# Optimization experiments

Measured on AMD Instinct MI355X. Metric: run time of the kernel, lower is better.

Reference implementation:

```python
import jax, jax.numpy as jnp
import numpy as np

D_MODEL = 1024
STATE_DIM = 256
BATCH = 4
SEQ_LEN = 4096


def setup_inputs() -> dict:
    key = jax.random.key(0)
    k_u, k_B, k_C = jax.random.split(key, 3)
    u = jax.random.normal(k_u, (BATCH, SEQ_LEN, D_MODEL), dtype=jnp.float32)
    # parameters (as in torch init)
    log_lambda = jnp.linspace(2.94, 4.6, STATE_DIM, dtype=jnp.float32)
    # nn.Linear weight shape is [out_features, in_features]
    B_w = jax.random.normal(k_B, (STATE_DIM, D_MODEL), dtype=jnp.float32) / np.sqrt(D_MODEL)
    C_w = jax.random.normal(k_C, (D_MODEL, STATE_DIM), dtype=jnp.float32) / np.sqrt(STATE_DIM)
    D = jnp.ones((D_MODEL,), dtype=jnp.float32)
    return {"u": u, "log_lambda": log_lambda, "B_w": B_w, "C_w": C_w, "D": D}


def reference(u, log_lambda, B_w, C_w, D):
    batch, seq_len, d = u.shape
    # Bu = B(u): [B, L, N]
    Bu = jnp.einsum("bld,nd->bln", u, B_w)
    lam = jax.nn.sigmoid(log_lambda)                     # [N]
    t = jnp.arange(seq_len, dtype=lam.dtype)
    kernel = lam[None, :] ** t[:, None]                  # [L, N]
    # next power of two >= 2*L (static)
    fft_len = 1
    while fft_len < 2 * seq_len:
        fft_len *= 2
    K_hat = jnp.fft.rfft(kernel, n=fft_len, axis=0)      # [F, N]
    Bu_hat = jnp.fft.rfft(Bu, n=fft_len, axis=1)         # [B, F, N]
    h_hat = K_hat[None, :, :] * Bu_hat
    h = jnp.fft.irfft(h_hat, n=fft_len, axis=1)[:, :seq_len, :]  # [B, L, N]
    y = jnp.einsum("bln,dn->bld", h, C_w) + D * u
    return y
```

## Files before the change

kernel.cpp:

```cpp
#include <hip/hip_runtime.h>
#include <hip/hip_bf16.h>

#define D_MODEL 1024
#define STATE_N 256
#define BATCH 4
#define SEQ_LEN 4096
#define M_TOTAL (BATCH * SEQ_LEN)
#define NCHUNK 128
#define CHUNK (SEQ_LEN / NCHUNK)

typedef __attribute__((ext_vector_type(8))) short bf16x8;
typedef __attribute__((ext_vector_type(4))) short s16x4;
typedef __attribute__((ext_vector_type(4))) float f32x4;

static __device__ inline short f2bf(float f) {
    union { float f; unsigned u; } v; v.f = f;
    unsigned r = v.u + 0x7FFFu + ((v.u >> 16) & 1u);
    return (short)(r >> 16);
}
static __device__ inline float bf2f(short s) {
    union { unsigned u; float f; } v;
    v.u = ((unsigned)(unsigned short)s) << 16;
    return v.f;
}
static __device__ inline float sigmoidf(float x) { return 1.0f / (1.0f + expf(-x)); }

#define GLOAD_LDS16(gp, lp)                                                     \
    __builtin_amdgcn_global_load_lds(                                           \
        (const __attribute__((address_space(1))) void*)(gp),                    \
        (__attribute__((address_space(3))) void*)(lp), 16, 0, 0)

#define WAITVM(N) asm volatile("s_waitcnt vmcnt(" #N ")" ::: "memory")
#define WAITLGKM0 asm volatile("s_waitcnt lgkmcnt(0)" ::: "memory")
#define BARRIER() do { __builtin_amdgcn_s_barrier(); asm volatile("" ::: "memory"); } while (0)

__global__ void prep(const float* __restrict__ Bw, const float* __restrict__ Cw,
                     const float* __restrict__ ll,
                     short* __restrict__ Bwt, short* __restrict__ Cwt,
                     float* __restrict__ W) {
    const int bx = blockIdx.x, tid = threadIdx.x;
    if (bx >= 256) {
        const int i = bx - 256, n = tid;
        W[i * 256 + n] = powf(sigmoidf(ll[n]), (float)(31 - i));
        return;
    }
    const int g = bx * 256 + tid;
    const float* s; short* d;
    if (g < 32768) {
        const int col = g & 127, kc = (g >> 7) & 7, kt = (g >> 10) & 15, cb = g >> 14;
        s = Bw + (size_t)(cb * 128 + col) * D_MODEL + kt * 64 + kc * 8;
        d = Bwt + (size_t)g * 8;
    } else {
        const int h = g - 32768;
        const int col = h & 63, ksq = (h >> 6) & 7, tt = (h >> 9) & 3, cb = h >> 11;
        s = Cw + (size_t)(cb * 64 + col) * STATE_N + tt * 64 + ksq * 8;
        d = Cwt + (size_t)h * 8;
    }
    const f32x4 v0 = *(const f32x4*)s;
    const f32x4 v1 = *(const f32x4*)(s + 4);
    bf16x8 r;
    #pragma unroll
    for (int q = 0; q < 4; ++q) { r[q] = f2bf(v0[q]); r[4 + q] = f2bf(v1[q]); }
    *(bf16x8*)d = r;
}

__global__ __launch_bounds__(256, 2) void gemm1(const float* __restrict__ u,
                                                const short* __restrict__ Bwt,
                                                const float* __restrict__ W,
                                                short* __restrict__ Bu,
                                                float* __restrict__ ends) {
    __shared__ short Ash[2][64 * 64];
    __shared__ short Bsh[3][8 * 128 * 8];
    const int tid = threadIdx.x;
    const int lane = tid & 63, wave = tid >> 6;
    const int lr = lane & 15, kq = lane >> 4;
    const int wr = wave >> 1, wc = wave & 1;
    const int wg = ((blockIdx.x & 7) << 6) + (blockIdx.x >> 3);
    const int cb = wg & 1, strip = wg >> 1;
    const int m0 = strip * 64, n0 = cb * 128;

    const int a_r = tid >> 4, a_k = (tid & 15) * 4;
    const float* au = u + (size_t)m0 * D_MODEL + (size_t)a_r * D_MODEL + a_k;
    const int a_ch = (tid & 15) >> 1, a_half = (tid & 1) * 4;
    const short* bg = Bwt + (size_t)cb * 16 * 8192;

    f32x4 acc[2][4] = {};
    f32x4 ar0[4], ar1[4], ar2[4];

    #define LOADA(SET, KT)                                                       \
        do { _Pragma("unroll")                                                   \
             for (int i = 0; i < 4; ++i)                                         \
                 SET[i] = *(const f32x4*)(au + (size_t)i * 16 * D_MODEL + (KT) * 64); } while (0)
    #define WRITEA(BUF, SET)                                                     \
        do { _Pragma("unroll")                                                   \
             for (int i = 0; i < 4; ++i) {                                       \
                 const int row = i * 16 + a_r;                                   \
                 s16x4 wv;                                                       \
                 _Pragma("unroll")                                               \
                 for (int e = 0; e < 4; ++e) wv[e] = f2bf(SET[i][e]);            \
                 *(s16x4*)&Ash[BUF][(row * 8 + (a_ch ^ (row & 7))) * 8 + a_half] = wv; \
             } } while (0)
    #define STAGEB(BUF, KT)                                                      \
        do { const short* bs = bg + (size_t)(KT) * 8192;                         \
             _Pragma("unroll")                                                   \
             for (int q = 0; q < 4; ++q)                                         \
                 GLOAD_LDS16(bs + (q * 256 + tid) * 8,                           \
                             (char*)&Bsh[BUF][0] + (q * 256 + wave * 64) * 16); } while (0)

    LOADA(ar0, 0);
    WAITVM(0);
    WRITEA(0, ar0);
    STAGEB(0, 0);
    LOADA(ar1, 1);
    STAGEB(1, 1);
    LOADA(ar2, 2);
    WAITLGKM0;

    #pragma unroll
    for (int t = 0; t < 16; ++t) {
        if (t < 14)      { WAITVM(8); }
        else if (t == 14){ WAITVM(4); }
        else             { WAITVM(0); }
        BARRIER();
        if (t < 15) {
            if (((t + 1) % 3) == 0)      WRITEA((t + 1) & 1, ar0);
            else if (((t + 1) % 3) == 1) WRITEA((t + 1) & 1, ar1);
            else                         WRITEA((t + 1) & 1, ar2);
        }
        bf16x8 af[2][2], bfr[2][4];
        #pragma unroll
        for (int ks = 0; ks < 2; ++ks) {
            #pragma unroll
            for (int i = 0; i < 2; ++i) {
                const int row = wr * 32 + i * 16 + lr;
                af[ks][i] = *(const bf16x8*)&Ash[t & 1][(row * 8 + ((ks * 4 + kq) ^ (row & 7))) * 8];
            }
            #pragma unroll
            for (int j = 0; j < 4; ++j)
                bfr[ks][j] = *(const bf16x8*)&Bsh[t % 3][((ks * 4 + kq) * 128 + wc * 64 + j * 16 + lr) * 8];
        }
        if (t + 2 <= 15) STAGEB((t + 2) % 3, t + 2);
        if (t + 3 <= 15) {
            if (((t + 3) % 3) == 0)      LOADA(ar0, t + 3);
            else if (((t + 3) % 3) == 1) LOADA(ar1, t + 3);
            else                         LOADA(ar2, t + 3);
        }
        #pragma unroll
        for (int ks = 0; ks < 2; ++ks)
            #pragma unroll
            for (int i = 0; i < 2; ++i)
                #pragma unroll
                for (int j = 0; j < 4; ++j)
                    acc[i][j] = __builtin_amdgcn_mfma_f32_16x16x32_bf16(bfr[ks][j], af[ks][i], acc[i][j], 0, 0, 0);
    }
    #undef LOADA
    #undef WRITEA
    #undef STAGEB

    #pragma unroll
    for (int i = 0; i < 2; ++i) {
        const int m = m0 + wr * 32 + i * 16 + lr;
        #pragma unroll
        for (int j = 0; j < 4; ++j) {
            const int n = n0 + wc * 64 + j * 16 + kq * 4;
            s16x4 st;
            #pragma unroll
            for (int r = 0; r < 4; ++r) st[r] = f2bf(acc[i][j][r]);
            *(s16x4*)(Bu + (size_t)m * STATE_N + n) = st;
        }
    }

    float part[4][4];
    #pragma unroll
    for (int j = 0; j < 4; ++j) {
        const int nb = n0 + wc * 64 + j * 16 + kq * 4;
        const f32x4 w0 = *(const f32x4*)(W + (size_t)lr * 256 + nb);
        const f32x4 w1 = *(const f32x4*)(W + (size_t)(16 + lr) * 256 + nb);
        #pragma unroll
        for (int r = 0; r < 4; ++r)
            part[j][r] = w0[r] * acc[0][j][r] + w1[r] * acc[1][j][r];
    }
    #pragma unroll
    for (int m = 1; m <= 8; m <<= 1)
        #pragma unroll
        for (int j = 0; j < 4; ++j)
            #pragma unroll
            for (int r = 0; r < 4; ++r)
                part[j][r] += __shfl_xor(part[j][r], m, 64);
    if (lr == 0) {
        const int cg = strip * 2 + wr;
        #pragma unroll
        for (int j = 0; j < 4; ++j) {
            f32x4 e;
            #pragma unroll
            for (int r = 0; r < 4; ++r) e[r] = part[j][r];
            *(f32x4*)(ends + (size_t)cg * STATE_N + n0 + wc * 64 + j * 16 + kq * 4) = e;
        }
    }
}

__global__ __launch_bounds__(256) void gemm2(const short* __restrict__ hbf,
                                             const short* __restrict__ Cwt,
                                             const float* __restrict__ u,
                                             const float* __restrict__ Dv,
                                             float* __restrict__ y) {
    __shared__ short Ash[4][64 * 64];
    __shared__ short Bsh[4][8 * 64 * 8];
    const int tid = threadIdx.x;
    const int lane = tid & 63, wave = tid >> 6;
    const int lr = lane & 15, kq = lane >> 4;
    const int wr = wave >> 1, wc = wave & 1;
    const int wg = ((blockIdx.x & 7) << 9) + (blockIdx.x >> 3);
    const int cb = wg & 15, strip = wg >> 4;
    const int m0 = strip * 64, n0 = cb * 64;

    const int aslot0 = wave * 128 + lane, aslot1 = aslot0 + 64;
    const int arow0 = aslot0 >> 3, arow1 = aslot1 >> 3;
    const int ac = lane & 7;
    const short* ag0 = hbf + (size_t)(m0 + arow0) * STATE_N + ((ac ^ (arow0 & 7)) << 3);
    const short* ag1 = hbf + (size_t)(m0 + arow1) * STATE_N + ((ac ^ (arow1 & 7)) << 3);
    const short* bg = Cwt + (size_t)cb * 4 * 8 * 64 * 8;

    #pragma unroll
    for (int t = 0; t < 4; ++t) {
        GLOAD_LDS16(ag0 + t * 64, (char*)&Ash[t][0] + aslot0 * 16);
        GLOAD_LDS16(ag1 + t * 64, (char*)&Ash[t][0] + aslot1 * 16);
        const short* bs = bg + (size_t)t * 4096;
        GLOAD_LDS16(bs + ((wave * 2 + 0) * 64 + lane) * 8,
                    (char*)&Bsh[t][0] + (wave * 128 + lane) * 16);
        GLOAD_LDS16(bs + ((wave * 2 + 1) * 64 + lane) * 8,
                    (char*)&Bsh[t][0] + (wave * 128 + 64 + lane) * 16);
    }

    f32x4 acc[2][2] = {};
    #pragma unroll
    for (int t = 0; t < 4; ++t) {
        if (t == 0)      { WAITVM(12); }
        else if (t == 1) { WAITVM(8); }
        else if (t == 2) { WAITVM(4); }
        else             { WAITVM(0); }
        BARRIER();
        bf16x8 af[2][2], bfr[2][2];
        #pragma unroll
        for (int ks = 0; ks < 2; ++ks) {
            #pragma unroll
            for (int i = 0; i < 2; ++i) {
                const int row = wr * 32 + i * 16 + lr;
                af[i][ks] = *(const bf16x8*)&Ash[t][row * 64 + ((((ks << 2) | kq) ^ (row & 7)) << 3)];
            }
            #pragma unroll
            for (int j = 0; j < 2; ++j)
                bfr[j][ks] = *(const bf16x8*)&Bsh[t][((ks << 2) | kq) * 512 + (wc * 32 + j * 16 + lr) * 8];
        }
        #pragma unroll
        for (int ks = 0; ks < 2; ++ks)
            #pragma unroll
            for (int i = 0; i < 2; ++i)
                #pragma unroll
                for (int j = 0; j < 2; ++j)
                    acc[i][j] = __builtin_amdgcn_mfma_f32_16x16x32_bf16(bfr[j][ks], af[i][ks], acc[i][j], 0, 0, 0);
    }

    #pragma unroll
    for (int i = 0; i < 2; ++i) {
        const int m = m0 + wr * 32 + i * 16 + lr;
        #pragma unroll
        for (int j = 0; j < 2; ++j) {
            const int n = n0 + wc * 32 + j * 16 + kq * 4;
            const size_t o = (size_t)m * D_MODEL + n;
            const f32x4 uv = *(const f32x4*)(u + o);
            const f32x4 dv = *(const f32x4*)(Dv + n);
            f32x4 rv;
            #pragma unroll
            for (int q = 0; q < 4; ++q) rv[q] = fmaf(dv[q], uv[q], acc[i][j][q]);
            *(f32x4*)(y + o) = rv;
        }
    }
}

__global__ void scan_carry(const float* __restrict__ ends,
                           const float* __restrict__ log_lambda,
                           float* __restrict__ carries) {
    const int n = threadIdx.x;
    const int b = blockIdx.x;
    const float lam = sigmoidf(log_lambda[n]);
    const float lamC = powf(lam, (float)CHUNK);
    float carry = 0.0f;
    #pragma unroll 16
    for (int c = 0; c < NCHUNK; ++c) {
        const size_t o = ((size_t)(b * NCHUNK + c)) * STATE_N + n;
        carries[o] = carry;
        carry = fmaf(lamC, carry, ends[o]);
    }
}

__global__ void scan_fix(const short* __restrict__ Bu,
                         const float* __restrict__ log_lambda,
                         const float* __restrict__ carries,
                         short* __restrict__ hbf) {
    const int wave = threadIdx.x >> 6, lane = threadIdx.x & 63;
    const int cg = blockIdx.x * 4 + wave;
    const int b = cg >> 7, c = cg & (NCHUNK - 1);
    const int n0 = lane * 4;
    float lam[4], h[4];
    #pragma unroll
    for (int q = 0; q < 4; ++q) lam[q] = sigmoidf(log_lambda[n0 + q]);
    const f32x4 cv = *(const f32x4*)(carries + (size_t)cg * STATE_N + n0);
    #pragma unroll
    for (int q = 0; q < 4; ++q) h[q] = cv[q];
    size_t idx = ((size_t)(b * SEQ_LEN + c * CHUNK)) * STATE_N + n0;
    #pragma unroll
    for (int i = 0; i < CHUNK; ++i) {
        const s16x4 v = *(const s16x4*)(Bu + idx);
        s16x4 o;
        #pragma unroll
        for (int q = 0; q < 4; ++q) { h[q] = fmaf(lam[q], h[q], bf2f(v[q])); o[q] = f2bf(h[q]); }
        *(s16x4*)(hbf + idx) = o;
        idx += STATE_N;
    }
}

extern "C" void kernel_launch(void* const* d_in, const int* in_sizes, int n_in,
                              void* d_out, int out_size, void* d_ws, size_t ws_size,
                              hipStream_t stream) {
    const float* u  = (const float*)d_in[0];
    const float* ll = (const float*)d_in[1];
    const float* Bw = (const float*)d_in[2];
    const float* Cw = (const float*)d_in[3];
    const float* Dv = (const float*)d_in[4];
    float* y = (float*)d_out;

    char* ws = (char*)d_ws;
    size_t off = 0;
    short* Bwt = (short*)(ws + off); off += (size_t)STATE_N * D_MODEL * 2;
    short* Cwt = (short*)(ws + off); off += (size_t)D_MODEL * STATE_N * 2;
    float* W   = (float*)(ws + off); off += (size_t)32 * STATE_N * 4;
    short* Bu  = (short*)(ws + off); off += (size_t)M_TOTAL * STATE_N * 2;
    short* hbf = (short*)(ws + off); off += (size_t)M_TOTAL * STATE_N * 2;
    float* ends = (float*)(ws + off); off += (size_t)BATCH * NCHUNK * STATE_N * 4;
    float* carries = (float*)(ws + off);

    prep<<<288, 256, 0, stream>>>(Bw, Cw, ll, Bwt, Cwt, W);
    gemm1<<<512, 256, 0, stream>>>(u, Bwt, W, Bu, ends);
    scan_carry<<<BATCH, STATE_N, 0, stream>>>(ends, ll, carries);
    scan_fix<<<BATCH * NCHUNK / 4, 256, 0, stream>>>(Bu, ll, carries, hbf);
    gemm2<<<4096, 256, 0, stream>>>(hbf, Cwt, u, Dv, y);
}
```

Measured before the change: 70.77 us.

## Fuse intra-chunk scan fix-up into gemm2 prologue via LDS

Removes the separate scan_fix kernel and its hbf buffer. Each gemm2 block now loads raw Bu tiles into LDS, applies the carry-seeded recurrence per chunk in shared memory, and then runs the MFMA GEMM. This drops one kernel launch and a full write and read of the intermediate h tensor. In exchange, the scan is recomputed redundantly across the 16 column blocks that share each strip, and the prologue adds serialized latency before the GEMM loop.

```diff
diff --git a/kernel.cpp b/kernel.cpp
--- a/kernel.cpp
+++ b/kernel.cpp
@@ -11,6 +11,7 @@
 
 typedef __attribute__((ext_vector_type(8))) short bf16x8;
 typedef __attribute__((ext_vector_type(4))) short s16x4;
+typedef __attribute__((ext_vector_type(2))) short s16x2;
 typedef __attribute__((ext_vector_type(4))) float f32x4;
 
 static __device__ inline short f2bf(float f) {
@@ -199,8 +200,10 @@
     }
 }
 
-__global__ __launch_bounds__(256) void gemm2(const short* __restrict__ hbf,
+__global__ __launch_bounds__(256) void gemm2(const short* __restrict__ Bu,
                                              const short* __restrict__ Cwt,
+                                             const float* __restrict__ ll,
+                                             const float* __restrict__ carries,
                                              const float* __restrict__ u,
                                              const float* __restrict__ Dv,
                                              float* __restrict__ y) {
@@ -214,17 +217,29 @@
     const int cb = wg & 15, strip = wg >> 4;
     const int m0 = strip * 64, n0 = cb * 64;
 
+    const int ch = tid >> 7;
+    const int cp = tid & 127;
+    const int st = cp >> 5;
+    const int c0 = (2 * cp) & 63;
+    const int scc = c0 >> 3, scw = c0 & 7;
+
+    const float2 lraw = *(const float2*)(ll + 2 * cp);
+    const float2 car2 = *(const float2*)(carries + (size_t)(strip * 2 + ch) * STATE_N + 2 * cp);
+
     const int aslot0 = wave * 128 + lane, aslot1 = aslot0 + 64;
     const int arow0 = aslot0 >> 3, arow1 = aslot1 >> 3;
     const int ac = lane & 7;
-    const short* ag0 = hbf + (size_t)(m0 + arow0) * STATE_N + ((ac ^ (arow0 & 7)) << 3);
-    const short* ag1 = hbf + (size_t)(m0 + arow1) * STATE_N + ((ac ^ (arow1 & 7)) << 3);
+    const short* ag0 = Bu + (size_t)(m0 + arow0) * STATE_N + ((ac ^ (arow0 & 7)) << 3);
+    const short* ag1 = Bu + (size_t)(m0 + arow1) * STATE_N + ((ac ^ (arow1 & 7)) << 3);
     const short* bg = Cwt + (size_t)cb * 4 * 8 * 64 * 8;
 
     #pragma unroll
     for (int t = 0; t < 4; ++t) {
         GLOAD_LDS16(ag0 + t * 64, (char*)&Ash[t][0] + aslot0 * 16);
         GLOAD_LDS16(ag1 + t * 64, (char*)&Ash[t][0] + aslot1 * 16);
+    }
+    #pragma unroll
+    for (int t = 0; t < 4; ++t) {
         const short* bs = bg + (size_t)t * 4096;
         GLOAD_LDS16(bs + ((wave * 2 + 0) * 64 + lane) * 8,
                     (char*)&Bsh[t][0] + (wave * 128 + lane) * 16);
@@ -232,12 +247,36 @@
                     (char*)&Bsh[t][0] + (wave * 128 + 64 + lane) * 16);
     }
 
+    WAITVM(8);
+    BARRIER();
+
+    {
+        const float lam0 = sigmoidf(lraw.x), lam1 = sigmoidf(lraw.y);
+        s16x2 rv[32];
+        #pragma unroll
+        for (int i = 0; i < 32; ++i)
+            rv[i] = *(const s16x2*)&Ash[st][(ch * 32 + i) * 64 + ((scc ^ (i & 7)) << 3) + scw];
+        float h0 = car2.x, h1 = car2.y;
+        #pragma unroll
+        for (int i = 0; i < 32; ++i) {
+            h0 = fmaf(lam0, h0, bf2f(rv[i][0]));
+            h1 = fmaf(lam1, h1, bf2f(rv[i][1]));
+            s16x2 o; o[0] = f2bf(h0); o[1] = f2bf(h1);
+            rv[i] = o;
+        }
+        #pragma unroll
+        for (int i = 0; i < 32; ++i)
+            *(s16x2*)&Ash[st][(ch * 32 + i) * 64 + ((scc ^ (i & 7)) << 3) + scw] = rv[i];
+    }
+    WAITLGKM0;
+    BARRIER();
+
     f32x4 acc[2][2] = {};
     #pragma unroll
     for (int t = 0; t < 4; ++t) {
-        if (t == 0)      { WAITVM(12); }
-        else if (t == 1) { WAITVM(8); }
-        else if (t == 2) { WAITVM(4); }
+        if (t == 0)      { WAITVM(6); }
+        else if (t == 1) { WAITVM(4); }
+        else if (t == 2) { WAITVM(2); }
         else             { WAITVM(0); }
         BARRIER();
         bf16x8 af[2][2], bfr[2][2];
@@ -294,32 +333,6 @@
     }
 }
 
-__global__ void scan_fix(const short* __restrict__ Bu,
-                         const float* __restrict__ log_lambda,
-                         const float* __restrict__ carries,
-                         short* __restrict__ hbf) {
-    const int wave = threadIdx.x >> 6, lane = threadIdx.x & 63;
-    const int cg = blockIdx.x * 4 + wave;
-    const int b = cg >> 7, c = cg & (NCHUNK - 1);
-    const int n0 = lane * 4;
-    float lam[4], h[4];
-    #pragma unroll
-    for (int q = 0; q < 4; ++q) lam[q] = sigmoidf(log_lambda[n0 + q]);
-    const f32x4 cv = *(const f32x4*)(carries + (size_t)cg * STATE_N + n0);
-    #pragma unroll
-    for (int q = 0; q < 4; ++q) h[q] = cv[q];
-    size_t idx = ((size_t)(b * SEQ_LEN + c * CHUNK)) * STATE_N + n0;
-    #pragma unroll
-    for (int i = 0; i < CHUNK; ++i) {
-        const s16x4 v = *(const s16x4*)(Bu + idx);
-        s16x4 o;
-        #pragma unroll
-        for (int q = 0; q < 4; ++q) { h[q] = fmaf(lam[q], h[q], bf2f(v[q])); o[q] = f2bf(h[q]); }
-        *(s16x4*)(hbf + idx) = o;
-        idx += STATE_N;
-    }
-}
-
 extern "C" void kernel_launch(void* const* d_in, const int* in_sizes, int n_in,
                               void* d_out, int out_size, void* d_ws, size_t ws_size,
                               hipStream_t stream) {
@@ -336,13 +349,11 @@
     short* Cwt = (short*)(ws + off); off += (size_t)D_MODEL * STATE_N * 2;
     float* W   = (float*)(ws + off); off += (size_t)32 * STATE_N * 4;
     short* Bu  = (short*)(ws + off); off += (size_t)M_TOTAL * STATE_N * 2;
-    short* hbf = (short*)(ws + off); off += (size_t)M_TOTAL * STATE_N * 2;
     float* ends = (float*)(ws + off); off += (size_t)BATCH * NCHUNK * STATE_N * 4;
     float* carries = (float*)(ws + off);
 
     prep<<<288, 256, 0, stream>>>(Bw, Cw, ll, Bwt, Cwt, W);
     gemm1<<<512, 256, 0, stream>>>(u, Bwt, W, Bu, ends);
     scan_carry<<<BATCH, STATE_N, 0, stream>>>(ends, ll, carries);
-    scan_fix<<<BATCH * NCHUNK / 4, 256, 0, stream>>>(Bu, ll, carries, hbf);
-    gemm2<<<4096, 256, 0, stream>>>(hbf, Cwt, u, Dv, y);
-}
+    gemm2<<<4096, 256, 0, stream>>>(Bu, Cwt, ll, carries, u, Dv, y);
+}
```

Result: no change. 71.75 us (+1.4%).
